# Performance work log

Measured on AMD Instinct MI355X. Metric: run time of the kernel, lower is better.

The kernel has to match this reference:

```python
import jax, jax.numpy as jnp
import numpy as np

N_NODES = 50000
N_EDGES = 800000
IN_CH, HID, OUT_CH = 128, 256, 40


def setup_inputs() -> dict:
    key = jax.random.key(0)
    ks = jax.random.split(key, 10)
    x = jax.random.normal(ks[0], (N_NODES, IN_CH), dtype=jnp.float32)
    edge_index = jax.random.randint(ks[1], (2, N_EDGES), 0, N_NODES, dtype=jnp.int64)
    s = 0.05  # weight init scale
    return {
        "x": x,
        "edge_index": edge_index,
        "W1a": jax.random.normal(ks[2], (IN_CH, HID), dtype=jnp.float32) * s,
        "b1a": jnp.zeros((HID,), jnp.float32),
        "W2a": jax.random.normal(ks[3], (HID, HID), dtype=jnp.float32) * s,
        "b2a": jnp.zeros((HID,), jnp.float32),
        "W1b": jax.random.normal(ks[4], (HID, HID), dtype=jnp.float32) * s,
        "b1b": jnp.zeros((HID,), jnp.float32),
        "W2b": jax.random.normal(ks[5], (HID, HID), dtype=jnp.float32) * s,
        "b2b": jnp.zeros((HID,), jnp.float32),
        "Wlin": jax.random.normal(ks[6], (HID * 2, OUT_CH), dtype=jnp.float32) * s,
        "blin": jnp.zeros((OUT_CH,), jnp.float32),
    }


def _gin_conv(h, src, dst, W1, b1, W2, b2):
    # sum-aggregate messages h[src] into destination nodes, eps = 0
    agg = jax.ops.segment_sum(h[src], dst, num_segments=N_NODES)
    z = h + agg
    z = jnp.maximum(z @ W1 + b1, 0.0) @ W2 + b2  # 2-layer MLP
    return z


def reference(x, edge_index, W1a, b1a, W2a, b2a, W1b, b1b, W2b, b2b, Wlin, blin):
    src, dst = edge_index[0], edge_index[1]
    h1 = jnp.maximum(_gin_conv(x, src, dst, W1a, b1a, W2a, b2a), 0.0)
    h2 = jnp.maximum(_gin_conv(h1, src, dst, W1b, b1b, W2b, b2b), 0.0)
    h_cat = jnp.concatenate([h1, h2], axis=1)  # [N, 2*HID]
    logits = h_cat @ Wlin + blin
    return jax.nn.log_softmax(logits, axis=1)
```

## Files before the change

kernel.cpp:

```cpp
#include <hip/hip_runtime.h>
#include <math.h>

#define N_NODES 50000
#define N_EDGES 800000
#define IN_CH 128
#define HID 256
#define OUT_CH 40
#define GRP 6250
#define HGRP 3125
#define NCHUNK 32
#define TS 264

typedef unsigned short u16;
typedef unsigned char u8;
typedef __attribute__((ext_vector_type(8))) short bf16x8;
typedef __attribute__((ext_vector_type(8))) unsigned short u16x8;
typedef __attribute__((ext_vector_type(4))) float f32x4;
typedef __attribute__((ext_vector_type(2))) float f32x2;

__device__ __forceinline__ float bf2f(u16 u) {
    union { unsigned int i; float f; } v; v.i = ((unsigned int)u) << 16; return v.f;
}
__device__ __forceinline__ u16 f2bf(float f) {
    union { float f; unsigned int i; } v; v.f = f;
    unsigned int x = v.i;
    x += 0x7fffu + ((x >> 16) & 1u);
    return (u16)(x >> 16);
}

#define GLOBAL_AS __attribute__((address_space(1)))
#define LDS_AS __attribute__((address_space(3)))
__device__ __forceinline__ void async_cp16(const void* g, void* l) {
    __builtin_amdgcn_global_load_lds((const GLOBAL_AS unsigned int*)g,
                                     (LDS_AS unsigned int*)l, 16, 0, 0);
}

__device__ __forceinline__ void pack_w(
    const float* __restrict__ in, u16* __restrict__ out, int K, int N, int c)
{
    for (int k = threadIdx.x; k < K; k += 256) {
        int kk32 = k >> 5, quad = (k >> 3) & 3, e = k & 7;
        size_t base = (((size_t)c * (K >> 5) + kk32) * 64 + quad * 16) * 8 + e;
#pragma unroll
        for (int li = 0; li < 16; li++) {
            int n = c * 16 + li;
            float v = (n < N) ? in[(size_t)k * N + n] : 0.f;
            out[base + (size_t)li * 8] = f2bf(v);
        }
    }
}

__global__ __launch_bounds__(256) void prep_fused(
    const float* __restrict__ x, u16* __restrict__ xb, u8* __restrict__ xf8,
    const int* __restrict__ ei, u16* __restrict__ e16,
    const float* __restrict__ W1a, const float* __restrict__ W2a,
    const float* __restrict__ W1b, const float* __restrict__ W2b,
    const float* __restrict__ Wlin,
    u16* __restrict__ W1aPk, u16* __restrict__ W2aPk,
    u16* __restrict__ W1bPk, u16* __restrict__ W2bPk, u16* __restrict__ WlinPk)
{
    int b = blockIdx.x;
    if (b < 6250) {
        int i = b * 256 + threadIdx.x;
        float4 v = ((const float4*)x)[i];
        ushort4 o;
        o.x = f2bf(v.x); o.y = f2bf(v.y); o.z = f2bf(v.z); o.w = f2bf(v.w);
        ((ushort4*)xb)[i] = o;
        int p = __builtin_amdgcn_cvt_pk_fp8_f32(v.x, v.y, 0, false);
        p = __builtin_amdgcn_cvt_pk_fp8_f32(v.z, v.w, p, true);
        ((unsigned int*)xf8)[i] = (unsigned int)p;
    } else if (b < 7813) {
        int i = (b - 6250) * 256 + threadIdx.x;
        if (i < (2 * N_EDGES) / 4) {
            int4 v = ((const int4*)ei)[i];
            ushort4 o;
            o.x = (u16)v.x; o.y = (u16)v.y; o.z = (u16)v.z; o.w = (u16)v.w;
            ((ushort4*)e16)[i] = o;
        }
    } else {
        int t = b - 7813;
        if (t < 16)       pack_w(W1a, W1aPk, IN_CH, HID, t);
        else if (t < 32)  pack_w(W2a, W2aPk, HID, HID, t - 16);
        else if (t < 48)  pack_w(W1b, W1bPk, HID, HID, t - 32);
        else if (t < 64)  pack_w(W2b, W2bPk, HID, HID, t - 48);
        else              pack_w(Wlin, WlinPk, 2 * HID, OUT_CH, t - 64);
    }
}

__global__ __launch_bounds__(256) void hist_priv(
    const u16* __restrict__ dst16, u16* __restrict__ partial)
{
    __shared__ int hist[HGRP];
    const int b = blockIdx.x;
    const int gh = b & 15;
    const int sub = b >> 4;
    const int lo = gh * HGRP;
    const int CH = N_EDGES / NCHUNK;
    for (int i = threadIdx.x; i < HGRP; i += 256) hist[i] = 0;
    __syncthreads();
    const ushort4* dsts = (const ushort4*)(dst16 + sub * CH);
    for (int k = threadIdx.x; k < CH / 4; k += 256) {
        ushort4 d = dsts[k];
        int r0 = (int)d.x - lo, r1 = (int)d.y - lo;
        int r2 = (int)d.z - lo, r3 = (int)d.w - lo;
        if ((unsigned)r0 < (unsigned)HGRP) atomicAdd(&hist[r0], 1);
        if ((unsigned)r1 < (unsigned)HGRP) atomicAdd(&hist[r1], 1);
        if ((unsigned)r2 < (unsigned)HGRP) atomicAdd(&hist[r2], 1);
        if ((unsigned)r3 < (unsigned)HGRP) atomicAdd(&hist[r3], 1);
    }
    __syncthreads();
    u16* po = partial + (size_t)(sub * 8 + (gh >> 1)) * GRP + (gh & 1) * HGRP;
    for (int i = threadIdx.x; i < HGRP; i += 256) po[i] = (u16)hist[i];
}

__global__ __launch_bounds__(256) void deg_cp(
    const u16* __restrict__ partial, u16* __restrict__ chunkpref,
    u16* __restrict__ deg16)
{
    int node = blockIdx.x * 256 + threadIdx.x;
    if (node >= N_NODES) return;
    int g = node / GRP;
    int off = node - g * GRP;
    int d = 0;
#pragma unroll
    for (int sub = 0; sub < NCHUNK; sub++) {
        chunkpref[(size_t)sub * N_NODES + node] = (u16)d;
        d += partial[(size_t)(sub * 8 + g) * GRP + off];
    }
    deg16[node] = (u16)d;
}

__global__ __launch_bounds__(256) void scan1(
    const u16* __restrict__ deg16, int* __restrict__ excl,
    int* __restrict__ partials_out)
{
    __shared__ int lds[256];
    const int tid = threadIdx.x;
    const int base = blockIdx.x * 1024 + tid * 4;
    int v[4]; int s = 0;
#pragma unroll
    for (int i = 0; i < 4; i++) {
        int idx = base + i;
        int d = (idx < N_NODES) ? (int)deg16[idx] : 0;
        v[i] = d;
        s += d;
    }
    lds[tid] = s;
    __syncthreads();
    for (int off = 1; off < 256; off <<= 1) {
        int t = (tid >= off) ? lds[tid - off] : 0;
        __syncthreads();
        lds[tid] += t;
        __syncthreads();
    }
    int run = lds[tid] - s;
#pragma unroll
    for (int i = 0; i < 4; i++) {
        int idx = base + i;
        if (idx < N_NODES) excl[idx] = run;
        run += v[i];
    }
    if (tid == 255) partials_out[blockIdx.x] = lds[255];
}

__global__ __launch_bounds__(256) void scan3(
    int* __restrict__ excl, const int* __restrict__ partials,
    int* __restrict__ sentinel, int nPart)
{
    __shared__ int bp[64];
    const int tid = threadIdx.x;
    if (tid < 64) {
        int orig = (tid < nPart) ? partials[tid] : 0;
        int v = orig;
#pragma unroll
        for (int off = 1; off < 64; off <<= 1) {
            int t = __shfl_up(v, off, 64);
            if (tid >= off) v += t;
        }
        bp[tid] = v - orig;
    }
    __syncthreads();
    int idx = blockIdx.x * 256 + tid;
    if (idx < N_NODES) {
        int r = excl[idx] + bp[idx >> 10];
        excl[idx] = r;
    }
    if (idx == 0) sentinel[0] = N_EDGES;
}

__global__ __launch_bounds__(256) void csr_fill(
    const u16* __restrict__ src16, const u16* __restrict__ dst16,
    const int* __restrict__ rowp, const u16* __restrict__ chunkpref,
    u16* __restrict__ csr_src)
{
    __shared__ int cur[HGRP];
    const int gh = blockIdx.x & 15;
    const int c = blockIdx.x >> 4;
    const int lo = gh * HGRP;
    const int CH = N_EDGES / NCHUNK;
    const u16* cp = chunkpref + (size_t)c * N_NODES + lo;
    for (int i = threadIdx.x; i < HGRP; i += 256)
        cur[i] = rowp[lo + i] + cp[i];
    __syncthreads();
    const ushort4* dsts = (const ushort4*)(dst16 + c * CH);
    const ushort4* srcs = (const ushort4*)(src16 + c * CH);
    for (int k = threadIdx.x; k < CH / 4; k += 256) {
        ushort4 d = dsts[k];
        ushort4 sc = srcs[k];
        int r0 = (int)d.x - lo, r1 = (int)d.y - lo;
        int r2 = (int)d.z - lo, r3 = (int)d.w - lo;
        if ((unsigned)r0 < (unsigned)HGRP) { int p = atomicAdd(&cur[r0], 1); csr_src[p] = sc.x; }
        if ((unsigned)r1 < (unsigned)HGRP) { int p = atomicAdd(&cur[r1], 1); csr_src[p] = sc.y; }
        if ((unsigned)r2 < (unsigned)HGRP) { int p = atomicAdd(&cur[r2], 1); csr_src[p] = sc.z; }
        if ((unsigned)r3 < (unsigned)HGRP) { int p = atomicAdd(&cur[r3], 1); csr_src[p] = sc.w; }
    }
}


__global__ __launch_bounds__(256) void gather_agg_f8_128(
    const u16* __restrict__ feat_bf, const u8* __restrict__ feat_f8,
    const int* __restrict__ row_ptr, const int* __restrict__ row_end,
    const u16* __restrict__ csr_src, u16* __restrict__ out)
{
    const int tid = threadIdx.x;
    const int lane = tid & 63;
    const int wv = tid >> 6;
    const int li = lane & 7;
    int node = blockIdx.x * 32 + wv * 8 + (lane >> 3);
    const bool valid = node < N_NODES;
    if (!valid) node = N_NODES - 1;

    int j = row_ptr[node];
    int deg = valid ? (row_end[node] - j) : 0;

    float acc[16];
    {
        u16x8 s0 = *(const u16x8*)(feat_bf + (size_t)node * IN_CH + li * 16);
        u16x8 s1 = *(const u16x8*)(feat_bf + (size_t)node * IN_CH + li * 16 + 8);
#pragma unroll
        for (int q = 0; q < 8; q++) { acc[q] = bf2f(s0[q]); acc[8 + q] = bf2f(s1[q]); }
    }

    int maxdeg = deg;
#pragma unroll
    for (int off = 8; off < 64; off <<= 1)
        maxdeg = max(maxdeg, __shfl_xor(maxdeg, off, 64));

    for (int it = 0; it < maxdeg; it += 4) {
        int4 g0 = {0,0,0,0}, g1 = {0,0,0,0}, g2 = {0,0,0,0}, g3 = {0,0,0,0};
        if (it < deg)
            g0 = *(const int4*)(feat_f8 + (size_t)csr_src[j + it] * IN_CH + li * 16);
        if (it + 1 < deg)
            g1 = *(const int4*)(feat_f8 + (size_t)csr_src[j + it + 1] * IN_CH + li * 16);
        if (it + 2 < deg)
            g2 = *(const int4*)(feat_f8 + (size_t)csr_src[j + it + 2] * IN_CH + li * 16);
        if (it + 3 < deg)
            g3 = *(const int4*)(feat_f8 + (size_t)csr_src[j + it + 3] * IN_CH + li * 16);
#pragma unroll
        for (int q = 0; q < 4; q++) {
            int w0 = (&g0.x)[q], w1 = (&g1.x)[q], w2 = (&g2.x)[q], w3 = (&g3.x)[q];
            f32x2 l0 = __builtin_amdgcn_cvt_pk_f32_fp8(w0, false);
            f32x2 h0 = __builtin_amdgcn_cvt_pk_f32_fp8(w0, true);
            f32x2 l1 = __builtin_amdgcn_cvt_pk_f32_fp8(w1, false);
            f32x2 h1 = __builtin_amdgcn_cvt_pk_f32_fp8(w1, true);
            f32x2 l2 = __builtin_amdgcn_cvt_pk_f32_fp8(w2, false);
            f32x2 h2 = __builtin_amdgcn_cvt_pk_f32_fp8(w2, true);
            f32x2 l3 = __builtin_amdgcn_cvt_pk_f32_fp8(w3, false);
            f32x2 h3 = __builtin_amdgcn_cvt_pk_f32_fp8(w3, true);
            acc[q * 4 + 0] += (l0.x + l1.x) + (l2.x + l3.x);
            acc[q * 4 + 1] += (l0.y + l1.y) + (l2.y + l3.y);
            acc[q * 4 + 2] += (h0.x + h1.x) + (h2.x + h3.x);
            acc[q * 4 + 3] += (h0.y + h1.y) + (h2.y + h3.y);
        }
    }

    if (valid) {
        u16x8 o0, o1;
#pragma unroll
        for (int q = 0; q < 8; q++) { o0[q] = f2bf(acc[q]); o1[q] = f2bf(acc[8 + q]); }
        *(u16x8*)(out + (size_t)node * IN_CH + li * 16) = o0;
        *(u16x8*)(out + (size_t)node * IN_CH + li * 16 + 8) = o1;
    }
}

__global__ __launch_bounds__(256) void gather_agg_f8_256(
    const u16* __restrict__ feat_bf, const u8* __restrict__ feat_f8,
    const int* __restrict__ row_ptr, const int* __restrict__ row_end,
    const u16* __restrict__ csr_src, u16* __restrict__ out)
{
    const int tid = threadIdx.x;
    const int lane = tid & 63;
    const int wv = tid >> 6;
    const int li = lane & 15;
    const int node = blockIdx.x * 16 + wv * 4 + (lane >> 4);

    int j = row_ptr[node];
    int deg = row_end[node] - j;

    float acc[16];
    {
        u16x8 s0 = *(const u16x8*)(feat_bf + (size_t)node * HID + li * 16);
        u16x8 s1 = *(const u16x8*)(feat_bf + (size_t)node * HID + li * 16 + 8);
#pragma unroll
        for (int q = 0; q < 8; q++) { acc[q] = bf2f(s0[q]); acc[8 + q] = bf2f(s1[q]); }
    }

    int maxdeg = deg;
#pragma unroll
    for (int off = 16; off < 64; off <<= 1)
        maxdeg = max(maxdeg, __shfl_xor(maxdeg, off, 64));

    for (int it = 0; it < maxdeg; it += 4) {
        int4 g0 = {0,0,0,0}, g1 = {0,0,0,0}, g2 = {0,0,0,0}, g3 = {0,0,0,0};
        if (it < deg)
            g0 = *(const int4*)(feat_f8 + (size_t)csr_src[j + it] * HID + li * 16);
        if (it + 1 < deg)
            g1 = *(const int4*)(feat_f8 + (size_t)csr_src[j + it + 1] * HID + li * 16);
        if (it + 2 < deg)
            g2 = *(const int4*)(feat_f8 + (size_t)csr_src[j + it + 2] * HID + li * 16);
        if (it + 3 < deg)
            g3 = *(const int4*)(feat_f8 + (size_t)csr_src[j + it + 3] * HID + li * 16);
#pragma unroll
        for (int q = 0; q < 4; q++) {
            int w0 = (&g0.x)[q], w1 = (&g1.x)[q], w2 = (&g2.x)[q], w3 = (&g3.x)[q];
            f32x2 l0 = __builtin_amdgcn_cvt_pk_f32_fp8(w0, false);
            f32x2 h0 = __builtin_amdgcn_cvt_pk_f32_fp8(w0, true);
            f32x2 l1 = __builtin_amdgcn_cvt_pk_f32_fp8(w1, false);
            f32x2 h1 = __builtin_amdgcn_cvt_pk_f32_fp8(w1, true);
            f32x2 l2 = __builtin_amdgcn_cvt_pk_f32_fp8(w2, false);
            f32x2 h2 = __builtin_amdgcn_cvt_pk_f32_fp8(w2, true);
            f32x2 l3 = __builtin_amdgcn_cvt_pk_f32_fp8(w3, false);
            f32x2 h3 = __builtin_amdgcn_cvt_pk_f32_fp8(w3, true);
            acc[q * 4 + 0] += (l0.x + l1.x) + (l2.x + l3.x);
            acc[q * 4 + 1] += (l0.y + l1.y) + (l2.y + l3.y);
            acc[q * 4 + 2] += (h0.x + h1.x) + (h2.x + h3.x);
            acc[q * 4 + 3] += (h0.y + h1.y) + (h2.y + h3.y);
        }
    }

    u16x8 o0, o1;
#pragma unroll
    for (int q = 0; q < 8; q++) { o0[q] = f2bf(acc[q]); o1[q] = f2bf(acc[8 + q]); }
    *(u16x8*)(out + (size_t)node * HID + li * 16) = o0;
    *(u16x8*)(out + (size_t)node * HID + li * 16 + 8) = o1;
}

__global__ __launch_bounds__(256, 4) void mlp_fused(
    const u16* __restrict__ A, int K1,
    const u16* __restrict__ W1pk, const float* __restrict__ b1,
    const u16* __restrict__ W2pk, const float* __restrict__ b2,
    u16* __restrict__ out, u8* __restrict__ outF8, int M)
{
    __shared__ u16 SB[64 * TS];

    const int tid = threadIdx.x;
    const int lane = tid & 63;
    const int wid = tid >> 6;
    const int li = lane & 15;
    const int quad = lane >> 4;
    const int koff = quad * 8;
    const int row0 = blockIdx.x * 64;
    const int KB1 = K1 >> 5;
    const int rsh = (K1 == 256) ? 9 : 8;

    {
        const u8* Ag = (const u8*)(A + (size_t)row0 * K1);
        const int rounds = K1 >> 5;
        for (int j = 0; j < rounds; j++) {
            int L = (j * 256 + tid) * 16;
            int G = L ^ (((L >> rsh) & 7) << 4);
            async_cp16(Ag + G, (u8*)SB + L);
        }
    }

    f32x4 acc[4][4];
#pragma unroll
    for (int i = 0; i < 4; i++)
#pragma unroll
        for (int j = 0; j < 4; j++) acc[i][j] = (f32x4){0.f, 0.f, 0.f, 0.f};

#define LDW(WF, WPK, KB, KK32)                                                \
    {   _Pragma("unroll")                                                     \
        for (int t = 0; t < 4; t++)                                           \
            WF[t] = *(const bf16x8*)((WPK) +                                  \
                (((size_t)(wid * 4 + t) * (KB) + (KK32)) * 64 + lane) * 8); }
#define LDA1(AF, KK)                                                          \
    {   _Pragma("unroll")                                                     \
        for (int t = 0; t < 4; t++) {                                         \
            int row = t * 16 + li;                                            \
            int bo = row * (K1 * 2) + ((KK) + koff) * 2;                      \
            bo ^= (row & 7) << 4;                                             \
            AF[t] = *(const bf16x8*)((const u8*)SB + bo); } }
#define LDA2(AF, KK)                                                          \
    {   _Pragma("unroll")                                                     \
        for (int t = 0; t < 4; t++)                                           \
            AF[t] = *(const bf16x8*)(SB + (t * 16 + li) * TS + (KK) + koff); }
#define MFMA16(AF, WF)                                                        \
    {   _Pragma("unroll")                                                     \
        for (int mt = 0; mt < 4; mt++)                                        \
            _Pragma("unroll")                                                 \
            for (int nt = 0; nt < 4; nt++)                                    \
                acc[mt][nt] = __builtin_amdgcn_mfma_f32_16x16x32_bf16(        \
                    AF[mt], WF[nt], acc[mt][nt], 0, 0, 0); }

    bf16x8 wfA[4], wfB[4], af[4];

    LDW(wfA, W1pk, KB1, 0);
    __syncthreads();

    for (int kk32 = 0; kk32 < KB1; kk32 += 2) {
        LDW(wfB, W1pk, KB1, kk32 + 1);
        LDA1(af, kk32 * 32);
        MFMA16(af, wfA);
        if (kk32 + 2 < KB1) LDW(wfA, W1pk, KB1, kk32 + 2);
        LDA1(af, kk32 * 32 + 32);
        MFMA16(af, wfB);
    }
    __syncthreads();

#pragma unroll
    for (int nt = 0; nt < 4; nt++) {
        int col = wid * 64 + nt * 16 + li;
        float bv = b1[col];
#pragma unroll
        for (int mt = 0; mt < 4; mt++) {
#pragma unroll
            for (int reg = 0; reg < 4; reg++) {
                int row = mt * 16 + quad * 4 + reg;
                float v = fmaxf(acc[mt][nt][reg] + bv, 0.f);
                SB[row * TS + col] = f2bf(v);
                acc[mt][nt][reg] = 0.f;
            }
        }
    }
    LDW(wfA, W2pk, 8, 0);
    __syncthreads();

    for (int kk32 = 0; kk32 < 8; kk32 += 2) {
        LDW(wfB, W2pk, 8, kk32 + 1);
        LDA2(af, kk32 * 32);
        MFMA16(af, wfA);
        if (kk32 + 2 < 8) LDW(wfA, W2pk, 8, kk32 + 2);
        LDA2(af, kk32 * 32 + 32);
        MFMA16(af, wfB);
    }
#undef LDW
#undef LDA1
#undef LDA2
#undef MFMA16

    __syncthreads();
#pragma unroll
    for (int nt = 0; nt < 4; nt++) {
        int col = wid * 64 + nt * 16 + li;
        float bv = b2[col];
#pragma unroll
        for (int mt = 0; mt < 4; mt++) {
#pragma unroll
            for (int reg = 0; reg < 4; reg++) {
                int row = mt * 16 + quad * 4 + reg;
                float v = fmaxf(acc[mt][nt][reg] + bv, 0.f);
                SB[row * TS + col] = f2bf(v);
            }
        }
    }
    __syncthreads();
#pragma unroll
    for (int it = 0; it < 8; it++) {
        int flat = it * 4096 + tid * 16;
        int r = flat >> 9;
        int cu = (flat & 511) >> 1;
        int row = row0 + r;
        if (row < M) {
            u16x8 v = *(const u16x8*)(SB + r * TS + cu);
            *(u16x8*)(out + (size_t)row * HID + cu) = v;
            if (outF8 != nullptr) {
                int p0 = __builtin_amdgcn_cvt_pk_fp8_f32(bf2f(v[0]), bf2f(v[1]), 0, false);
                p0 = __builtin_amdgcn_cvt_pk_fp8_f32(bf2f(v[2]), bf2f(v[3]), p0, true);
                int p1 = __builtin_amdgcn_cvt_pk_fp8_f32(bf2f(v[4]), bf2f(v[5]), 0, false);
                p1 = __builtin_amdgcn_cvt_pk_fp8_f32(bf2f(v[6]), bf2f(v[7]), p1, true);
                int2 pv; pv.x = p0; pv.y = p1;
                *(int2*)(outF8 + (size_t)row * HID + cu) = pv;
            }
        }
    }
}

__global__ __launch_bounds__(256, 6) void gemm_mfma(
    const u16* __restrict__ A, const u16* __restrict__ Acat, int Ksplit, int ldA,
    const u16* __restrict__ Bpk, const float* __restrict__ bias,
    float* __restrict__ out, int M, int K)
{
    const int tid = threadIdx.x;
    const int lane = tid & 63;
    const int wid = tid >> 6;
    const int li = lane & 15;
    const int quad = lane >> 4;
    const int koff = quad * 8;
    const int row0 = blockIdx.x * 64 + wid * 16;

    f32x4 acc[3];
#pragma unroll
    for (int i = 0; i < 3; i++) acc[i] = (f32x4){0.f, 0.f, 0.f, 0.f};

    int r = row0 + li;
    const int arow = (r < M) ? r : (M - 1);
    const int KB = K >> 5;

#define LD_G(AF, BF, KK)                                                      \
    {   const u16* Ab = ((KK) >= Ksplit) ? Acat : A;                          \
        const int kb = ((KK) >= Ksplit) ? ((KK) - Ksplit) : (KK);             \
        AF = *(const bf16x8*)(Ab + (size_t)arow * ldA + kb + koff);           \
        _Pragma("unroll")                                                     \
        for (int t = 0; t < 3; t++)                                           \
            BF[t] = *(const bf16x8*)(Bpk +                                    \
                (((size_t)t * KB + ((KK) >> 5)) * 64 + lane) * 8); }
#define MFMA3(AF, BF)                                                         \
    {   _Pragma("unroll")                                                     \
        for (int nt = 0; nt < 3; nt++)                                        \
            acc[nt] = __builtin_amdgcn_mfma_f32_16x16x32_bf16(                \
                AF, BF[nt], acc[nt], 0, 0, 0); }

    {
        bf16x8 a0, b0[3], a1, b1v[3];
        LD_G(a0, b0, 0);
        for (int kk = 0; kk < K; kk += 64) {
            LD_G(a1, b1v, kk + 32);
            MFMA3(a0, b0);
            if (kk + 64 < K) LD_G(a0, b0, kk + 64);
            MFMA3(a1, b1v);
        }
    }
#undef LD_G
#undef MFMA3

    float b0v = bias[li];
    float b1s = bias[16 + li];
    float b2s = (li < 8) ? bias[32 + li] : 0.f;
#pragma unroll
    for (int reg = 0; reg < 4; reg++) {
        int row = row0 + quad * 4 + reg;
        float v0 = acc[0][reg] + b0v;
        float v1 = acc[1][reg] + b1s;
        float v2 = (li < 8) ? (acc[2][reg] + b2s) : -INFINITY;
        float m = fmaxf(fmaxf(v0, v1), v2);
#pragma unroll
        for (int off = 1; off < 16; off <<= 1)
            m = fmaxf(m, __shfl_xor(m, off, 64));
        float s = expf(v0 - m) + expf(v1 - m)
                + ((li < 8) ? expf(v2 - m) : 0.f);
#pragma unroll
        for (int off = 1; off < 16; off <<= 1)
            s += __shfl_xor(s, off, 64);
        float lg = m + logf(s);
        if (row < M) {
            out[(size_t)row * OUT_CH + li] = v0 - lg;
            out[(size_t)row * OUT_CH + 16 + li] = v1 - lg;
            if (li < 8) out[(size_t)row * OUT_CH + 32 + li] = v2 - lg;
        }
    }
}

extern "C" void kernel_launch(void* const* d_in, const int* in_sizes, int n_in,
                              void* d_out, int out_size, void* d_ws, size_t ws_size,
                              hipStream_t stream)
{
    const float* x    = (const float*)d_in[0];
    const int*   ei   = (const int*)d_in[1];
    const float* W1a  = (const float*)d_in[2];
    const float* b1a  = (const float*)d_in[3];
    const float* W2a  = (const float*)d_in[4];
    const float* b2a  = (const float*)d_in[5];
    const float* W1b  = (const float*)d_in[6];
    const float* b1b  = (const float*)d_in[7];
    const float* W2b  = (const float*)d_in[8];
    const float* b2b  = (const float*)d_in[9];
    const float* Wlin = (const float*)d_in[10];
    const float* blin = (const float*)d_in[11];
    float* out = (float*)d_out;

    const size_t R = (size_t)N_NODES * HID;
    u16* R0 = (u16*)d_ws;
    u16* R1 = R0 + R;
    u16* R2 = R1 + R;
    u16* R3 = R2 + R;
    u16* R4 = R3 + R;
    u16* xbf = R0;
    u16* zA  = R1;
    u16* partial = (u16*)R1;
    u8*  xf8 = (u8*)(R1 + (size_t)N_NODES * IN_CH);
    u8*  h1f8 = (u8*)R1;
    u16* h1  = R3;
    u16* zB  = R4;
    u16* h2  = R2;

    u16* wts = R4 + R;
    u16* W1aPk = wts;
    u16* W2aPk = W1aPk + 256 * 128;
    u16* W1bPk = W2aPk + 256 * 256;
    u16* W2bPk = W1bPk + 256 * 256;
    u16* WlinPk = W2bPk + 256 * 256;
    int* rowp   = (int*)(WlinPk + 128 * 512);
    int* cursor = rowp + N_NODES;
    int* part   = cursor + N_NODES;
    u16* csr    = (u16*)(part + 64);
    u16* e16    = csr + N_EDGES;
    u16* src16  = e16;
    u16* dst16  = e16 + N_EDGES;
    u16* chunkpref = dst16 + N_EDGES;
    u16* deg16  = chunkpref + (size_t)NCHUNK * N_NODES;

    dim3 blk(256);
    const int scanBlocks = (N_NODES + 1023) / 1024;
    const int degBlocks  = (N_NODES + 255) / 256;
    const int agg128Blocks = (N_NODES + 31) / 32;
    const int agg256Blocks = N_NODES / 16;
    const int mlpBlocks  = (N_NODES + 63) / 64;
    const int gemmBlocks = (N_NODES + 63) / 64;

    prep_fused<<<7880, blk, 0, stream>>>(x, xbf, xf8, ei, e16,
                                         W1a, W2a, W1b, W2b, Wlin,
                                         W1aPk, W2aPk, W1bPk, W2bPk, WlinPk);
    hist_priv<<<16 * NCHUNK, blk, 0, stream>>>(dst16, partial);
    deg_cp<<<degBlocks, blk, 0, stream>>>(partial, chunkpref, deg16);
    scan1<<<scanBlocks, blk, 0, stream>>>(deg16, rowp, part);
    scan3<<<(N_NODES + 255) / 256, blk, 0, stream>>>(rowp, part, cursor, scanBlocks);
    csr_fill<<<16 * NCHUNK, blk, 0, stream>>>(src16, dst16, rowp, chunkpref, csr);

    gather_agg_f8_128<<<agg128Blocks, blk, 0, stream>>>(xbf, xf8, rowp, rowp + 1, csr, zA);
    mlp_fused<<<mlpBlocks, blk, 0, stream>>>(zA, IN_CH, W1aPk, b1a, W2aPk, b2a,
                                             h1, h1f8, N_NODES);

    gather_agg_f8_256<<<agg256Blocks, blk, 0, stream>>>(h1, h1f8, rowp, rowp + 1, csr, zB);
    mlp_fused<<<mlpBlocks, blk, 0, stream>>>(zB, HID, W1bPk, b1b, W2bPk, b2b,
                                             h2, nullptr, N_NODES);

    gemm_mfma<<<gemmBlocks, blk, 0, stream>>>(h1, h2, HID, HID, WlinPk, blin,
                                              out, N_NODES, 2 * HID);
}
```

Measured before the change: 260.4 us.

## Fold histogram into prep kernel and merge degree pass into scan

The per-chunk destination histogram now runs as extra blocks of the prep kernel, reading the int64-derived int32 edge indices directly, so it no longer waits on the 16-bit edge conversion. The degree/chunk-prefix kernel is merged into the first scan pass, now one node per thread, and the second scan pass runs a 256-wide block-prefix scan. This cuts the CSR build from five launches to three and removes the deg16 buffer. The trade-offs are a larger shared-memory footprint for every prep block, which may lower occupancy, and a redundant partials scan in each scan3 block.

```diff
diff --git a/kernel.cpp b/kernel.cpp
--- a/kernel.cpp
+++ b/kernel.cpp
@@ -57,8 +57,10 @@
     const float* __restrict__ W1b, const float* __restrict__ W2b,
     const float* __restrict__ Wlin,
     u16* __restrict__ W1aPk, u16* __restrict__ W2aPk,
-    u16* __restrict__ W1bPk, u16* __restrict__ W2bPk, u16* __restrict__ WlinPk)
-{
+    u16* __restrict__ W1bPk, u16* __restrict__ W2bPk, u16* __restrict__ WlinPk,
+    u16* __restrict__ partial)
+{
+    __shared__ int hist[HGRP];
     int b = blockIdx.x;
     if (b < 6250) {
         int i = b * 256 + threadIdx.x;
@@ -77,75 +79,55 @@
             o.x = (u16)v.x; o.y = (u16)v.y; o.z = (u16)v.z; o.w = (u16)v.w;
             ((ushort4*)e16)[i] = o;
         }
-    } else {
+    } else if (b < 7880) {
         int t = b - 7813;
         if (t < 16)       pack_w(W1a, W1aPk, IN_CH, HID, t);
         else if (t < 32)  pack_w(W2a, W2aPk, HID, HID, t - 16);
         else if (t < 48)  pack_w(W1b, W1bPk, HID, HID, t - 32);
         else if (t < 64)  pack_w(W2b, W2bPk, HID, HID, t - 48);
         else              pack_w(Wlin, WlinPk, 2 * HID, OUT_CH, t - 64);
-    }
-}
-
-__global__ __launch_bounds__(256) void hist_priv(
-    const u16* __restrict__ dst16, u16* __restrict__ partial)
-{
-    __shared__ int hist[HGRP];
-    const int b = blockIdx.x;
-    const int gh = b & 15;
-    const int sub = b >> 4;
-    const int lo = gh * HGRP;
-    const int CH = N_EDGES / NCHUNK;
-    for (int i = threadIdx.x; i < HGRP; i += 256) hist[i] = 0;
-    __syncthreads();
-    const ushort4* dsts = (const ushort4*)(dst16 + sub * CH);
-    for (int k = threadIdx.x; k < CH / 4; k += 256) {
-        ushort4 d = dsts[k];
-        int r0 = (int)d.x - lo, r1 = (int)d.y - lo;
-        int r2 = (int)d.z - lo, r3 = (int)d.w - lo;
-        if ((unsigned)r0 < (unsigned)HGRP) atomicAdd(&hist[r0], 1);
-        if ((unsigned)r1 < (unsigned)HGRP) atomicAdd(&hist[r1], 1);
-        if ((unsigned)r2 < (unsigned)HGRP) atomicAdd(&hist[r2], 1);
-        if ((unsigned)r3 < (unsigned)HGRP) atomicAdd(&hist[r3], 1);
-    }
-    __syncthreads();
-    u16* po = partial + (size_t)(sub * 8 + (gh >> 1)) * GRP + (gh & 1) * HGRP;
-    for (int i = threadIdx.x; i < HGRP; i += 256) po[i] = (u16)hist[i];
-}
-
-__global__ __launch_bounds__(256) void deg_cp(
+    } else {
+        const int hb = b - 7880;
+        const int gh = hb & 15;
+        const int sub = hb >> 4;
+        const int lo = gh * HGRP;
+        const int CH = N_EDGES / NCHUNK;
+        for (int i = threadIdx.x; i < HGRP; i += 256) hist[i] = 0;
+        __syncthreads();
+        const int4* dsts = (const int4*)(ei + N_EDGES + sub * CH);
+        for (int k = threadIdx.x; k < CH / 4; k += 256) {
+            int4 d = dsts[k];
+            int r0 = d.x - lo, r1 = d.y - lo;
+            int r2 = d.z - lo, r3 = d.w - lo;
+            if ((unsigned)r0 < (unsigned)HGRP) atomicAdd(&hist[r0], 1);
+            if ((unsigned)r1 < (unsigned)HGRP) atomicAdd(&hist[r1], 1);
+            if ((unsigned)r2 < (unsigned)HGRP) atomicAdd(&hist[r2], 1);
+            if ((unsigned)r3 < (unsigned)HGRP) atomicAdd(&hist[r3], 1);
+        }
+        __syncthreads();
+        u16* po = partial + (size_t)(sub * 8 + (gh >> 1)) * GRP + (gh & 1) * HGRP;
+        for (int i = threadIdx.x; i < HGRP; i += 256) po[i] = (u16)hist[i];
+    }
+}
+
+__global__ __launch_bounds__(256) void scan1(
     const u16* __restrict__ partial, u16* __restrict__ chunkpref,
-    u16* __restrict__ deg16)
-{
-    int node = blockIdx.x * 256 + threadIdx.x;
-    if (node >= N_NODES) return;
-    int g = node / GRP;
-    int off = node - g * GRP;
-    int d = 0;
-#pragma unroll
-    for (int sub = 0; sub < NCHUNK; sub++) {
-        chunkpref[(size_t)sub * N_NODES + node] = (u16)d;
-        d += partial[(size_t)(sub * 8 + g) * GRP + off];
-    }
-    deg16[node] = (u16)d;
-}
-
-__global__ __launch_bounds__(256) void scan1(
-    const u16* __restrict__ deg16, int* __restrict__ excl,
-    int* __restrict__ partials_out)
+    int* __restrict__ excl, int* __restrict__ partials_out)
 {
     __shared__ int lds[256];
     const int tid = threadIdx.x;
-    const int base = blockIdx.x * 1024 + tid * 4;
-    int v[4]; int s = 0;
-#pragma unroll
-    for (int i = 0; i < 4; i++) {
-        int idx = base + i;
-        int d = (idx < N_NODES) ? (int)deg16[idx] : 0;
-        v[i] = d;
-        s += d;
-    }
-    lds[tid] = s;
+    const int node = blockIdx.x * 256 + tid;
+    int d = 0;
+    if (node < N_NODES) {
+        int g = node / GRP;
+        int off = node - g * GRP;
+#pragma unroll
+        for (int sub = 0; sub < NCHUNK; sub++) {
+            chunkpref[(size_t)sub * N_NODES + node] = (u16)d;
+            d += partial[(size_t)(sub * 8 + g) * GRP + off];
+        }
+    }
+    lds[tid] = d;
     __syncthreads();
     for (int off = 1; off < 256; off <<= 1) {
         int t = (tid >= off) ? lds[tid - off] : 0;
@@ -153,13 +135,7 @@
         lds[tid] += t;
         __syncthreads();
     }
-    int run = lds[tid] - s;
-#pragma unroll
-    for (int i = 0; i < 4; i++) {
-        int idx = base + i;
-        if (idx < N_NODES) excl[idx] = run;
-        run += v[i];
-    }
+    if (node < N_NODES) excl[node] = lds[tid] - d;
     if (tid == 255) partials_out[blockIdx.x] = lds[255];
 }
 
@@ -167,24 +143,22 @@
     int* __restrict__ excl, const int* __restrict__ partials,
     int* __restrict__ sentinel, int nPart)
 {
-    __shared__ int bp[64];
+    __shared__ int lds[256];
+    __shared__ int bp[256];
     const int tid = threadIdx.x;
-    if (tid < 64) {
-        int orig = (tid < nPart) ? partials[tid] : 0;
-        int v = orig;
-#pragma unroll
-        for (int off = 1; off < 64; off <<= 1) {
-            int t = __shfl_up(v, off, 64);
-            if (tid >= off) v += t;
-        }
-        bp[tid] = v - orig;
-    }
-    __syncthreads();
-    int idx = blockIdx.x * 256 + tid;
-    if (idx < N_NODES) {
-        int r = excl[idx] + bp[idx >> 10];
-        excl[idx] = r;
-    }
+    int orig = (tid < nPart) ? partials[tid] : 0;
+    lds[tid] = orig;
+    __syncthreads();
+    for (int off = 1; off < 256; off <<= 1) {
+        int t = (tid >= off) ? lds[tid - off] : 0;
+        __syncthreads();
+        lds[tid] += t;
+        __syncthreads();
+    }
+    bp[tid] = lds[tid] - orig;
+    __syncthreads();
+    const int idx = blockIdx.x * 256 + tid;
+    if (idx < N_NODES) excl[idx] += bp[blockIdx.x];
     if (idx == 0) sentinel[0] = N_EDGES;
 }
 
@@ -601,30 +575,26 @@
     u16* W2bPk = W1bPk + 256 * 256;
     u16* WlinPk = W2bPk + 256 * 256;
     int* rowp   = (int*)(WlinPk + 128 * 512);
-    int* cursor = rowp + N_NODES;
-    int* part   = cursor + N_NODES;
-    u16* csr    = (u16*)(part + 64);
+    int* part   = rowp + N_NODES + 64;
+    u16* csr    = (u16*)(part + 256);
     u16* e16    = csr + N_EDGES;
     u16* src16  = e16;
     u16* dst16  = e16 + N_EDGES;
     u16* chunkpref = dst16 + N_EDGES;
-    u16* deg16  = chunkpref + (size_t)NCHUNK * N_NODES;
 
     dim3 blk(256);
-    const int scanBlocks = (N_NODES + 1023) / 1024;
-    const int degBlocks  = (N_NODES + 255) / 256;
+    const int scanBlocks = (N_NODES + 255) / 256;
     const int agg128Blocks = (N_NODES + 31) / 32;
     const int agg256Blocks = N_NODES / 16;
     const int mlpBlocks  = (N_NODES + 63) / 64;
     const int gemmBlocks = (N_NODES + 63) / 64;
 
-    prep_fused<<<7880, blk, 0, stream>>>(x, xbf, xf8, ei, e16,
+    prep_fused<<<8392, blk, 0, stream>>>(x, xbf, xf8, ei, e16,
                                          W1a, W2a, W1b, W2b, Wlin,
-                                         W1aPk, W2aPk, W1bPk, W2bPk, WlinPk);
-    hist_priv<<<16 * NCHUNK, blk, 0, stream>>>(dst16, partial);
-    deg_cp<<<degBlocks, blk, 0, stream>>>(partial, chunkpref, deg16);
-    scan1<<<scanBlocks, blk, 0, stream>>>(deg16, rowp, part);
-    scan3<<<(N_NODES + 255) / 256, blk, 0, stream>>>(rowp, part, cursor, scanBlocks);
+                                         W1aPk, W2aPk, W1bPk, W2bPk, WlinPk,
+                                         partial);
+    scan1<<<scanBlocks, blk, 0, stream>>>(partial, chunkpref, rowp, part);
+    scan3<<<scanBlocks, blk, 0, stream>>>(rowp, part, rowp + N_NODES, scanBlocks);
     csr_fill<<<16 * NCHUNK, blk, 0, stream>>>(src16, dst16, rowp, chunkpref, csr);
 
     gather_agg_f8_128<<<agg128Blocks, blk, 0, stream>>>(xbf, xf8, rowp, rowp + 1, csr, zA);
```

Result: faster. 252.1 us (-3.2%).
